# Kernel optimization log

Measured on AMD Instinct MI355X. Metric: run time of the kernel, lower is better.

## Reference

```python
import jax, jax.numpy as jnp
import numpy as np

NUM_HEADS = 8  # from init_kwargs


def setup_inputs() -> dict:
    key = jax.random.key(0)
    ks = jax.random.split(key, 8)
    B, N, Din, H, Dout, E = 4, 2048, 256, 512, 256, 65536
    s = 0.02
    return {
        "x": jax.random.normal(ks[0], (B, N, Din), jnp.float32),
        "edge_index": jax.random.randint(ks[1], (2, E), 0, N),
        "W_gcn": jax.random.normal(ks[2], (Din, H), jnp.float32) * s,
        "b_gcn": jnp.zeros((H,), jnp.float32),
        "in_proj_w": jax.random.normal(ks[3], (3 * H, H), jnp.float32) * s,
        "in_proj_b": jnp.zeros((3 * H,), jnp.float32),
        "out_proj_w": jax.random.normal(ks[4], (H, H), jnp.float32) * s,
        "out_proj_b": jnp.zeros((H,), jnp.float32),
        "fc_w": jax.random.normal(ks[5], (H, Dout), jnp.float32) * s,
        "fc_b": jnp.zeros((Dout,), jnp.float32),
    }


def _gcn(x, edge_index, W, b):
    # PyG GCNConv: add self-loops, symmetric normalization, gather-scatter aggregation.
    B, N, _ = x.shape
    loop = jnp.arange(N)
    src = jnp.concatenate([edge_index[0], loop])  # message source j
    dst = jnp.concatenate([edge_index[1], loop])  # aggregation target i
    deg = jnp.zeros((N,), x.dtype).at[dst].add(1.0)
    dinv = jnp.where(deg > 0, jax.lax.rsqrt(deg), 0.0)
    norm = dinv[src] * dinv[dst]                  # [Etot]
    xl = x @ W                                    # [B, N, H]
    msgs = xl[:, src, :] * norm[None, :, None]    # [B, Etot, H]
    out = jnp.zeros_like(xl).at[:, dst].add(msgs)  # scatter-add over edges
    return out + b


def _mha(x_nbh, wi, bi, wo, bo, nh):
    # torch MultiheadAttention, input [N(seq), B, H], self-attention.
    N, B, H = x_nbh.shape
    dh = H // nh
    qkv = x_nbh @ wi.T + bi                       # [N, B, 3H]
    q, k, v = jnp.split(qkv, 3, axis=-1)
    q = q.reshape(N, B, nh, dh) * (dh ** -0.5)
    k = k.reshape(N, B, nh, dh)
    v = v.reshape(N, B, nh, dh)
    scores = jnp.einsum("nbhd,mbhd->bhnm", q, k)  # [B, nh, N, N]
    attn = jax.nn.softmax(scores, axis=-1)
    o = jnp.einsum("bhnm,mbhd->nbhd", attn, v).reshape(N, B, H)
    return o @ wo.T + bo


def reference(x, edge_index, W_gcn, b_gcn, in_proj_w, in_proj_b,
              out_proj_w, out_proj_b, fc_w, fc_b):
    h = _gcn(x, edge_index, W_gcn, b_gcn)         # [B, N, H]
    h = jnp.transpose(h, (1, 0, 2))               # [N, B, H]
    h = _mha(h, in_proj_w, in_proj_b, out_proj_w, out_proj_b, NUM_HEADS)
    h = jnp.transpose(h, (1, 0, 2))               # [B, N, H]
    h = jax.nn.relu(h)
    return h @ fc_w + fc_b                        # [B, N, Dout]
```

## Files before the change

### kernel.cpp

```cpp
#include <hip/hip_runtime.h>
#include <hip/hip_bf16.h>


#define NN 2048
#define HH 512
#define NHEAD 8
#define DH 64

typedef _Float16 f16;
typedef __attribute__((ext_vector_type(2))) _Float16 f16x2;
typedef __attribute__((ext_vector_type(4))) _Float16 f16x4;
typedef __attribute__((ext_vector_type(8))) _Float16 f16x8;
typedef __attribute__((ext_vector_type(4))) float f32x4;

#define GLOAD_LDS16(g, l)                                              \
  __builtin_amdgcn_global_load_lds(                                    \
      (const __attribute__((address_space(1))) void*)(g),              \
      (__attribute__((address_space(3))) void*)(l), 16, 0, 0)


__global__ __launch_bounds__(256) void prep_cvt_kernel(const float* __restrict__ wi,
                                                       const float* __restrict__ wo,
                                                       f16* __restrict__ wi16,
                                                       f16* __restrict__ wo16,
                                                       float* __restrict__ deg,
                                                       int* __restrict__ cursor) {
  const int bid = blockIdx.x, t = threadIdx.x;
  if (bid < 768) {
    const int i = bid * 256 + t;
    const float4 v = ((const float4*)wi)[i];
    f16x4 o = { (f16)v.x, (f16)v.y, (f16)v.z, (f16)v.w };
    ((f16x4*)wi16)[i] = o;
  } else if (bid < 1024) {
    const int i = (bid - 768) * 256 + t;
    const float4 v = ((const float4*)wo)[i];
    f16x4 o = { (f16)v.x, (f16)v.y, (f16)v.z, (f16)v.w };
    ((f16x4*)wo16)[i] = o;
  } else {
    for (int i = t; i < NN; i += 256) { deg[i] = 1.0f; cursor[i] = 0; }
  }
}

__global__ __launch_bounds__(256) void prep_transpose_kernel(const float* __restrict__ wg,
                                                             const float* __restrict__ fcw,
                                                             f16* __restrict__ wg16t,
                                                             f16* __restrict__ fcw16t) {
  __shared__ float tbuf[32][33];
  const float* in;
  f16* outp;
  int R, C, bx, by;
  if (blockIdx.x < 128) { in = wg;  outp = wg16t;  R = 256; C = 512;
                          bx = blockIdx.x & 15; by = blockIdx.x >> 4; }
  else { int id = blockIdx.x - 128; in = fcw; outp = fcw16t; R = 512; C = 256;
         bx = id & 7; by = id >> 3; }
  const int c0 = bx * 32, r0 = by * 32;
  const int tx = threadIdx.x & 31, ty = threadIdx.x >> 5;
#pragma unroll
  for (int i = 0; i < 32; i += 8) tbuf[ty + i][tx] = in[(size_t)(r0 + ty + i) * C + c0 + tx];
  __syncthreads();
#pragma unroll
  for (int i = 0; i < 32; i += 8)
    outp[(size_t)(c0 + ty + i) * R + r0 + tx] = (f16)tbuf[tx][ty + i];
}


__global__ __launch_bounds__(256) void count_deg_kernel(const int* __restrict__ ei, int E,
                                                        float* __restrict__ deg) {
  int e = blockIdx.x * 256 + threadIdx.x;
  if (e < E) atomicAdd(&deg[ei[E + e]], 1.0f);
}

__global__ __launch_bounds__(1024) void build_rowptr_kernel(const float* __restrict__ deg,
                                                            float* __restrict__ dinv,
                                                            int* __restrict__ rowptr) {
  __shared__ int a[NN];
  __shared__ int bbuf[NN];
  const int t = threadIdx.x;
  for (int i = t; i < NN; i += 1024) {
    float dg = deg[i];
    a[i] = (int)dg - 1;
    dinv[i] = rsqrtf(dg);
  }
  __syncthreads();
  int* src = a;
  int* dst = bbuf;
  for (int off = 1; off < NN; off <<= 1) {
    for (int i = t; i < NN; i += 1024) {
      int v = src[i];
      if (i >= off) v += src[i - off];
      dst[i] = v;
    }
    __syncthreads();
    int* tmp = src; src = dst; dst = tmp;
  }
  for (int i = t; i < NN; i += 1024) rowptr[i + 1] = src[i];
  if (t == 0) rowptr[0] = 0;
}

__global__ __launch_bounds__(256) void fill_csr_kernel(const int* __restrict__ ei, int E,
                                                       const int* __restrict__ rowptr,
                                                       int* __restrict__ cursor,
                                                       int* __restrict__ csr_src) {
  int e = blockIdx.x * 256 + threadIdx.x;
  if (e < E) {
    int s = ei[e];
    int d = ei[E + e];
    int pos = atomicAdd(&cursor[d], 1);
    csr_src[rowptr[d] + pos] = s;
  }
}


template <int OUTMODE, bool BIAS, bool RELU, bool AF32, int MT = 128>
__global__ __launch_bounds__(256) void mfma_gemm_kernel(
    const void* __restrict__ Ap, const f16* __restrict__ Bt,
    const float* __restrict__ bias, void* __restrict__ Cout,
    int M, int N, int K,
    f16* __restrict__ q_out, f16* __restrict__ k_out, f16* __restrict__ v_out) {
  constexpr int MI = MT / 32;
  __shared__ f16 As[MT * 32];
  __shared__ f16 Bs[128 * 32];
  const int tid = threadIdx.x;
  const int wave = tid >> 6, lane = tid & 63;
  const int quad = lane >> 4, l16 = lane & 15;
  const int m0 = blockIdx.y * MT, n0 = blockIdx.x * 128;
  const int moff = (wave >> 1) * (MI * 16), noff = (wave & 1) * 64;

  f32x4 acc[MI][4];
#pragma unroll
  for (int i = 0; i < MI; ++i)
#pragma unroll
    for (int j = 0; j < 4; ++j) acc[i][j] = (f32x4){0.f, 0.f, 0.f, 0.f};

  const int rpw = MT / 4;
  const int srowA = rpw * wave + (lane >> 2);
  const int srowB = 32 * wave + (lane >> 2);
  const int kch = (lane & 3) * 8;
  const f16* Ag = (const f16*)Ap + (size_t)(m0 + srowA) * K + kch;
  const float* Ag32 = (const float*)Ap + (size_t)(m0 + srowA) * K + kch;
  const f16* Bg = Bt + (size_t)(n0 + srowB) * K + kch;
  f16* As_w = &As[(rpw * wave) * 32];
  f16* Bs_w = &Bs[(32 * wave) * 32];

  for (int k0 = 0; k0 < K; k0 += 32) {
    __syncthreads();
    if (AF32) {
#pragma unroll
      for (int t = 0; t < 2; ++t) {
        const float* g = Ag32 + k0 + (size_t)(16 * t) * K;
        const float4 u0 = *(const float4*)g;
        const float4 u1 = *(const float4*)(g + 4);
        f16x8 o = { (f16)u0.x, (f16)u0.y, (f16)u0.z, (f16)u0.w,
                    (f16)u1.x, (f16)u1.y, (f16)u1.z, (f16)u1.w };
        *(f16x8*)&As[(srowA + 16 * t) * 32 + kch] = o;
      }
    } else {
      GLOAD_LDS16(Ag + k0, As_w);
      if (MT == 128) GLOAD_LDS16(Ag + k0 + (size_t)16 * K, As_w + 16 * 32);
    }
    GLOAD_LDS16(Bg + k0, Bs_w);
    GLOAD_LDS16(Bg + k0 + (size_t)16 * K, Bs_w + 16 * 32);
    __syncthreads();
    f16x8 af[MI], bf[4];
#pragma unroll
    for (int m16 = 0; m16 < MI; ++m16)
      af[m16] = *(const f16x8*)&As[(moff + m16 * 16 + l16) * 32 + quad * 8];
#pragma unroll
    for (int n16 = 0; n16 < 4; ++n16)
      bf[n16] = *(const f16x8*)&Bs[(noff + n16 * 16 + l16) * 32 + quad * 8];
#pragma unroll
    for (int m16 = 0; m16 < MI; ++m16)
#pragma unroll
      for (int n16 = 0; n16 < 4; ++n16)
        acc[m16][n16] =
            __builtin_amdgcn_mfma_f32_16x16x32_f16(af[m16], bf[n16], acc[m16][n16], 0, 0, 0);
  }

  float bv[4];
#pragma unroll
  for (int n16 = 0; n16 < 4; ++n16)
    bv[n16] = BIAS ? bias[n0 + noff + n16 * 16 + l16] : 0.f;

  if (OUTMODE == 2) {
    const int hblk = (n0 >> 6) + (wave & 1);
    const int which = hblk >> 3, h = hblk & 7;
    f16* dst = (which == 0) ? q_out : (which == 1) ? k_out : v_out;
    const float scale = (which == 0) ? 0.125f : 1.0f;
#pragma unroll
    for (int m16 = 0; m16 < MI; ++m16) {
#pragma unroll
      for (int r = 0; r < 4; ++r) {
        const int m = m0 + moff + m16 * 16 + quad * 4 + r;
        const int b = m >> 11, ns = m & 2047;
        f16* row = dst + ((size_t)(b * 8 + h) * NN + ns) * DH;
#pragma unroll
        for (int n16 = 0; n16 < 4; ++n16) {
          const int d = n16 * 16 + l16;
          row[d] = (f16)((acc[m16][n16][r] + bv[n16]) * scale);
        }
      }
    }
  } else {
#pragma unroll
    for (int m16 = 0; m16 < MI; ++m16) {
#pragma unroll
      for (int r = 0; r < 4; ++r) {
        const size_t row = (size_t)(m0 + moff + m16 * 16 + quad * 4 + r) * N;
#pragma unroll
        for (int n16 = 0; n16 < 4; ++n16) {
          const int col = n0 + noff + n16 * 16 + l16;
          float v = acc[m16][n16][r] + bv[n16];
          if (RELU) v = fmaxf(v, 0.f);
          if (OUTMODE == 0) ((float*)Cout)[row + col] = v;
          else ((f16*)Cout)[row + col] = (f16)v;
        }
      }
    }
  }
}


__global__ __launch_bounds__(256) void gcn_aggregate_kernel(const f16* __restrict__ xl,
                                                            const float* __restrict__ dinv,
                                                            const int* __restrict__ rowptr,
                                                            const int* __restrict__ csr_src,
                                                            const float* __restrict__ b_gcn,
                                                            f16* __restrict__ out) {
  __shared__ int s_src[256];
  __shared__ float s_dv[256];
  const int i = blockIdx.x;
  const int tid = threadIdx.x;
  const int b = tid >> 6;
  const int f = (tid & 63) * 8;
  const float dv_i = dinv[i];
  const f16* xb = xl + (size_t)b * NN * HH;
  float acc[8];
  {
    const f16x8 self = *(const f16x8*)&xb[(size_t)i * HH + f];
#pragma unroll
    for (int c = 0; c < 8; ++c) acc[c] = (float)self[c] * dv_i;
  }
  const int beg = rowptr[i], end = rowptr[i + 1];
  for (int c0 = beg; c0 < end; c0 += 256) {
    const int cnt = min(256, end - c0);
    __syncthreads();
    if (tid < cnt) {
      int s = csr_src[c0 + tid];
      s_src[tid] = s;
      s_dv[tid] = dinv[s];
    }
    __syncthreads();
    for (int t = 0; t < cnt; ++t) {
      const f16x8 v = *(const f16x8*)&xb[(size_t)s_src[t] * HH + f];
      const float w = s_dv[t];
#pragma unroll
      for (int c = 0; c < 8; ++c) acc[c] = fmaf((float)v[c], w, acc[c]);
    }
  }
  const float4 bg0 = *(const float4*)&b_gcn[f];
  const float4 bg1 = *(const float4*)&b_gcn[f + 4];
  f16x8 o;
  o[0] = (f16)(acc[0] * dv_i + bg0.x);
  o[1] = (f16)(acc[1] * dv_i + bg0.y);
  o[2] = (f16)(acc[2] * dv_i + bg0.z);
  o[3] = (f16)(acc[3] * dv_i + bg0.w);
  o[4] = (f16)(acc[4] * dv_i + bg1.x);
  o[5] = (f16)(acc[5] * dv_i + bg1.y);
  o[6] = (f16)(acc[6] * dv_i + bg1.z);
  o[7] = (f16)(acc[7] * dv_i + bg1.w);
  *(f16x8*)&out[((size_t)b * NN + i) * HH + f] = o;
}


__global__ __launch_bounds__(256) void flash_attn_f16_kernel(const f16* __restrict__ Qb,
                                                             const f16* __restrict__ Kb,
                                                             const f16* __restrict__ Vb,
                                                             f16* __restrict__ Op,
                                                             float* __restrict__ Lp) {
  const int LDK = 72;
  const int LDV = 136;
  __shared__ f16 Ks[128 * LDK];
  __shared__ f16 Vt[64 * LDV];
  const int tid = threadIdx.x;
  const int wave = tid >> 6, lane = tid & 63;
  const int quad = lane >> 4, l16 = lane & 15;
  const int n0 = blockIdx.x * 128;
  const int bh = blockIdx.y;
  const int kh = blockIdx.z;
  const int b = bh >> 3, h = bh & 7;
  const f16* kb = Kb + (size_t)bh * NN * DH;
  const f16* vb = Vb + (size_t)bh * NN * DH;

  f16x8 aq[2][2];
#pragma unroll
  for (int g = 0; g < 2; ++g) {
    const f16* qf = Qb + ((size_t)bh * NN + n0 + (wave + 4 * g) * 16 + l16) * DH + quad * 8;
    aq[g][0] = *(const f16x8*)qf;
    aq[g][1] = *(const f16x8*)(qf + 32);
  }

  float l_part[2] = {0.f, 0.f};
  f32x4 acc_o[2][4];
#pragma unroll
  for (int g = 0; g < 2; ++g)
#pragma unroll
    for (int n16 = 0; n16 < 4; ++n16) acc_o[g][n16] = (f32x4){0.f, 0.f, 0.f, 0.f};

  const int vdg = tid & 15, jbb = tid >> 4;

  for (int kt = kh * 8; kt < kh * 8 + 8; ++kt) {
    const int k0 = kt * 128;
    __syncthreads();
#pragma unroll
    for (int i = 0; i < 4; ++i) {
      int idx = tid + 256 * i;
      int r = idx >> 3, koff = (idx & 7) * 8;
      *(f16x8*)&Ks[r * LDK + koff] = *(const f16x8*)(kb + (size_t)(k0 + r) * DH + koff);
    }
#pragma unroll
    for (int cc = 0; cc < 2; ++cc) {
      const int jb = jbb + 16 * cc;
      const int sb4 = (jb >> 3) * 32 + (jb & 3) * 8 + ((jb >> 2) & 1) * 4;
      f16x4 vv[4];
#pragma unroll
      for (int i = 0; i < 4; ++i)
        vv[i] = *(const f16x4*)(vb + (size_t)(k0 + jb * 4 + i) * DH + vdg * 4);
#pragma unroll
      for (int c = 0; c < 4; ++c) {
        f16x4 o = { vv[0][c], vv[1][c], vv[2][c], vv[3][c] };
        *(f16x4*)&Vt[(vdg * 4 + c) * LDV + sb4] = o;
      }
    }
    __syncthreads();
#pragma unroll
    for (int p = 0; p < 4; ++p) {
      f32x4 sA[2][2];
#pragma unroll
      for (int t = 0; t < 2; ++t) {
        const f16x8 ak0 = *(const f16x8*)&Ks[(p * 32 + t * 16 + l16) * LDK + quad * 8];
        const f16x8 ak1 = *(const f16x8*)&Ks[(p * 32 + t * 16 + l16) * LDK + quad * 8 + 32];
#pragma unroll
        for (int g = 0; g < 2; ++g) {
          f32x4 s = {0.f, 0.f, 0.f, 0.f};
          s = __builtin_amdgcn_mfma_f32_16x16x32_f16(ak0, aq[g][0], s, 0, 0, 0);
          s = __builtin_amdgcn_mfma_f32_16x16x32_f16(ak1, aq[g][1], s, 0, 0, 0);
          sA[g][t] = s;
        }
      }
      f16x8 bvv[4];
#pragma unroll
      for (int n16 = 0; n16 < 4; ++n16)
        bvv[n16] = *(const f16x8*)&Vt[(n16 * 16 + l16) * LDV + p * 32 + quad * 8];
#pragma unroll
      for (int g = 0; g < 2; ++g) {
        f16x8 ap;
        float sum = 0.f;
#pragma unroll
        for (int t = 0; t < 2; ++t)
#pragma unroll
          for (int r = 0; r < 4; ++r) {
            const float e = __expf(sA[g][t][r]);
            sum += e;
            ap[t * 4 + r] = (f16)e;
          }
        l_part[g] += sum;
#pragma unroll
        for (int n16 = 0; n16 < 4; ++n16)
          acc_o[g][n16] = __builtin_amdgcn_mfma_f32_16x16x32_f16(ap, bvv[n16], acc_o[g][n16], 0, 0, 0);
      }
    }
  }
  f16* ohalf = Op + (size_t)kh * 4 * NN * HH;
#pragma unroll
  for (int g = 0; g < 2; ++g) {
    float lp = l_part[g];
    lp += __shfl_xor(lp, 16);
    lp += __shfl_xor(lp, 32);
    const int qrow = n0 + (wave + 4 * g) * 16;
    if (quad == 0) Lp[(size_t)(kh * 32 + bh) * NN + qrow + l16] = lp;
    f16* obase = ohalf + ((size_t)b * NN + qrow) * HH + h * DH;
#pragma unroll
    for (int r = 0; r < 4; ++r)
#pragma unroll
      for (int n16 = 0; n16 < 4; ++n16)
        obase[(size_t)(quad * 4 + r) * HH + n16 * 16 + l16] = (f16)acc_o[g][n16][r];
  }
}

__global__ __launch_bounds__(256) void attn_combine_kernel(const f16* __restrict__ Op,
                                                           const float* __restrict__ Lp,
                                                           f16* __restrict__ attn) {
  const int idx = blockIdx.x * 256 + threadIdx.x;
  const int row = idx >> 7, c4 = (idx & 127) * 4;
  const int h = c4 >> 6;
  const int b = row >> 11, n = row & 2047;
  const int bh = b * 8 + h;
  const float l = Lp[(size_t)bh * NN + n] + Lp[(size_t)(32 + bh) * NN + n];
  const float inv = 1.0f / l;
  const f16x4 a0 = *(const f16x4*)&Op[(size_t)row * HH + c4];
  const f16x4 a1 = *(const f16x4*)&Op[(size_t)(4 * NN + row) * HH + c4];
  f16x4 o;
#pragma unroll
  for (int c = 0; c < 4; ++c) o[c] = (f16)(((float)a0[c] + (float)a1[c]) * inv);
  *(f16x4*)&attn[(size_t)row * HH + c4] = o;
}


extern "C" void kernel_launch(void* const* d_in, const int* in_sizes, int n_in,
                              void* d_out, int out_size, void* d_ws, size_t ws_size,
                              hipStream_t stream) {
  const float* x     = (const float*)d_in[0];
  const int*   ei    = (const int*)d_in[1];
  const float* W_gcn = (const float*)d_in[2];
  const float* b_gcn = (const float*)d_in[3];
  const float* wi    = (const float*)d_in[4];
  const float* bi    = (const float*)d_in[5];
  const float* wo    = (const float*)d_in[6];
  const float* bo    = (const float*)d_in[7];
  const float* fcw   = (const float*)d_in[8];
  const float* fcb   = (const float*)d_in[9];
  float* out = (float*)d_out;
  const int E = in_sizes[1] / 2;
  const int M = 4 * NN;

  char* wsb = (char*)d_ws;
  const size_t MB = 1u << 20;
  f16* xl16   = (f16*)(wsb + 4 * MB);
  f16* hb16   = (f16*)(wsb + 12 * MB);
  f16* Opart  = (f16*)(wsb + 4 * MB);
  f16* Qb     = (f16*)(wsb + 20 * MB);
  f16* Kb     = (f16*)(wsb + 28 * MB);
  f16* Vb     = (f16*)(wsb + 36 * MB);
  f16* attn16 = (f16*)(wsb + 44 * MB);
  f16* proj16 = (f16*)(wsb + 52 * MB);
  f16* wi16   = (f16*)(wsb + 60 * MB);
  f16* wo16   = (f16*)(wsb + 62 * MB);
  f16* wg16t  = (f16*)(wsb + 63 * MB);
  f16* fcw16t = (f16*)(wsb + 64 * MB);
  float* deg  = (float*)(wsb + 65 * MB);
  float* dinv = deg + NN;
  int* rowptr = (int*)(dinv + NN);
  int* cursor = rowptr + 2080;
  int* csr    = cursor + NN;
  float* Lpart = (float*)(wsb + 66 * MB);

  prep_cvt_kernel<<<1025, 256, 0, stream>>>(wi, wo, wi16, wo16, deg, cursor);
  prep_transpose_kernel<<<256, 256, 0, stream>>>(W_gcn, fcw, wg16t, fcw16t);

  count_deg_kernel<<<(E + 255) / 256, 256, 0, stream>>>(ei, E, deg);
  build_rowptr_kernel<<<1, 1024, 0, stream>>>(deg, dinv, rowptr);
  fill_csr_kernel<<<(E + 255) / 256, 256, 0, stream>>>(ei, E, rowptr, cursor, csr);

  mfma_gemm_kernel<1, false, false, true><<<dim3(4, 64), 256, 0, stream>>>(
      x, wg16t, nullptr, xl16, M, 512, 256, nullptr, nullptr, nullptr);
  gcn_aggregate_kernel<<<NN, 256, 0, stream>>>(xl16, dinv, rowptr, csr, b_gcn, hb16);
  mfma_gemm_kernel<2, true, false, false><<<dim3(12, 64), 256, 0, stream>>>(
      hb16, wi16, bi, nullptr, M, 1536, 512, Qb, Kb, Vb);
  flash_attn_f16_kernel<<<dim3(NN / 128, 32, 2), 256, 0, stream>>>(Qb, Kb, Vb, Opart, Lpart);
  attn_combine_kernel<<<M * (HH / 4) / 256, 256, 0, stream>>>(Opart, Lpart, attn16);
  mfma_gemm_kernel<1, true, true, false><<<dim3(4, 64), 256, 0, stream>>>(
      attn16, wo16, bo, proj16, M, 512, 512, nullptr, nullptr, nullptr);
  mfma_gemm_kernel<0, true, false, false, 64><<<dim3(2, 128), 256, 0, stream>>>(
      proj16, fcw16t, fcb, out, M, 256, 512, nullptr, nullptr, nullptr);
}
```

Measured before the change: 263.9 us.

## Drop attention split-K and combine kernel, use exp2 with prescaled Q, smaller GEMM tiles

The flash attention kernel no longer splits the key range into two halves. Each block loops over all keys, normalizes by the row sum itself and writes the final f16 output, so the partial-output buffer and the separate combine kernel go away. The log2(e) factor is folded into the Q scale so exp2f replaces __expf, and probabilities are packed with cvt_pkrtz. Two GEMMs switch to 64-row tiles with twice as many blocks, trading per-block reuse for more parallelism, while attention has half as many blocks, each running twice as long.

```diff
diff --git a/kernel.cpp b/kernel.cpp
--- a/kernel.cpp
+++ b/kernel.cpp
@@ -11,6 +11,7 @@
 typedef __attribute__((ext_vector_type(2))) _Float16 f16x2;
 typedef __attribute__((ext_vector_type(4))) _Float16 f16x4;
 typedef __attribute__((ext_vector_type(8))) _Float16 f16x8;
+typedef __attribute__((ext_vector_type(2))) __fp16 fp16v2;
 typedef __attribute__((ext_vector_type(4))) float f32x4;
 
 #define GLOAD_LDS16(g, l)                                              \
@@ -146,7 +147,7 @@
     __syncthreads();
     if (AF32) {
 #pragma unroll
-      for (int t = 0; t < 2; ++t) {
+      for (int t = 0; t < (MT == 128 ? 2 : 1); ++t) {
         const float* g = Ag32 + k0 + (size_t)(16 * t) * K;
         const float4 u0 = *(const float4*)g;
         const float4 u1 = *(const float4*)(g + 4);
@@ -185,7 +186,7 @@
     const int hblk = (n0 >> 6) + (wave & 1);
     const int which = hblk >> 3, h = hblk & 7;
     f16* dst = (which == 0) ? q_out : (which == 1) ? k_out : v_out;
-    const float scale = (which == 0) ? 0.125f : 1.0f;
+    const float scale = (which == 0) ? 0.125f * 1.44269504f : 1.0f;
 #pragma unroll
     for (int m16 = 0; m16 < MI; ++m16) {
 #pragma unroll
@@ -275,8 +276,7 @@
 __global__ __launch_bounds__(256) void flash_attn_f16_kernel(const f16* __restrict__ Qb,
                                                              const f16* __restrict__ Kb,
                                                              const f16* __restrict__ Vb,
-                                                             f16* __restrict__ Op,
-                                                             float* __restrict__ Lp) {
+                                                             f16* __restrict__ out) {
   const int LDK = 72;
   const int LDV = 136;
   __shared__ f16 Ks[128 * LDK];
@@ -286,7 +286,6 @@
   const int quad = lane >> 4, l16 = lane & 15;
   const int n0 = blockIdx.x * 128;
   const int bh = blockIdx.y;
-  const int kh = blockIdx.z;
   const int b = bh >> 3, h = bh & 7;
   const f16* kb = Kb + (size_t)bh * NN * DH;
   const f16* vb = Vb + (size_t)bh * NN * DH;
@@ -308,7 +307,7 @@
 
   const int vdg = tid & 15, jbb = tid >> 4;
 
-  for (int kt = kh * 8; kt < kh * 8 + 8; ++kt) {
+  for (int kt = 0; kt < NN / 128; ++kt) {
     const int k0 = kt * 128;
     __syncthreads();
 #pragma unroll
@@ -353,56 +352,42 @@
         bvv[n16] = *(const f16x8*)&Vt[(n16 * 16 + l16) * LDV + p * 32 + quad * 8];
 #pragma unroll
       for (int g = 0; g < 2; ++g) {
-        f16x8 ap;
+        float e[8];
         float sum = 0.f;
 #pragma unroll
         for (int t = 0; t < 2; ++t)
 #pragma unroll
           for (int r = 0; r < 4; ++r) {
-            const float e = __expf(sA[g][t][r]);
-            sum += e;
-            ap[t * 4 + r] = (f16)e;
+            const float v = exp2f(sA[g][t][r]);
+            e[t * 4 + r] = v;
+            sum += v;
           }
         l_part[g] += sum;
+        union { f16x8 v8; fp16v2 p2[4]; } ap;
+#pragma unroll
+        for (int c = 0; c < 4; ++c)
+          ap.p2[c] = __builtin_amdgcn_cvt_pkrtz(e[2 * c], e[2 * c + 1]);
 #pragma unroll
         for (int n16 = 0; n16 < 4; ++n16)
-          acc_o[g][n16] = __builtin_amdgcn_mfma_f32_16x16x32_f16(ap, bvv[n16], acc_o[g][n16], 0, 0, 0);
-      }
-    }
-  }
-  f16* ohalf = Op + (size_t)kh * 4 * NN * HH;
+          acc_o[g][n16] = __builtin_amdgcn_mfma_f32_16x16x32_f16(ap.v8, bvv[n16], acc_o[g][n16], 0, 0, 0);
+      }
+    }
+  }
 #pragma unroll
   for (int g = 0; g < 2; ++g) {
     float lp = l_part[g];
     lp += __shfl_xor(lp, 16);
     lp += __shfl_xor(lp, 32);
-    const int qrow = n0 + (wave + 4 * g) * 16;
-    if (quad == 0) Lp[(size_t)(kh * 32 + bh) * NN + qrow + l16] = lp;
-    f16* obase = ohalf + ((size_t)b * NN + qrow) * HH + h * DH;
-#pragma unroll
-    for (int r = 0; r < 4; ++r)
+    f16* obase = out + ((size_t)b * NN + n0 + (wave + 4 * g) * 16) * HH + h * DH;
+#pragma unroll
+    for (int r = 0; r < 4; ++r) {
+      const float lr = __shfl(lp, (lane & 48) | (quad * 4 + r));
+      const float inv = 1.0f / lr;
 #pragma unroll
       for (int n16 = 0; n16 < 4; ++n16)
-        obase[(size_t)(quad * 4 + r) * HH + n16 * 16 + l16] = (f16)acc_o[g][n16][r];
-  }
-}
-
-__global__ __launch_bounds__(256) void attn_combine_kernel(const f16* __restrict__ Op,
-                                                           const float* __restrict__ Lp,
-                                                           f16* __restrict__ attn) {
-  const int idx = blockIdx.x * 256 + threadIdx.x;
-  const int row = idx >> 7, c4 = (idx & 127) * 4;
-  const int h = c4 >> 6;
-  const int b = row >> 11, n = row & 2047;
-  const int bh = b * 8 + h;
-  const float l = Lp[(size_t)bh * NN + n] + Lp[(size_t)(32 + bh) * NN + n];
-  const float inv = 1.0f / l;
-  const f16x4 a0 = *(const f16x4*)&Op[(size_t)row * HH + c4];
-  const f16x4 a1 = *(const f16x4*)&Op[(size_t)(4 * NN + row) * HH + c4];
-  f16x4 o;
-#pragma unroll
-  for (int c = 0; c < 4; ++c) o[c] = (f16)(((float)a0[c] + (float)a1[c]) * inv);
-  *(f16x4*)&attn[(size_t)row * HH + c4] = o;
+        obase[(size_t)(quad * 4 + r) * HH + n16 * 16 + l16] = (f16)(acc_o[g][n16][r] * inv);
+    }
+  }
 }
 
 
@@ -427,7 +412,6 @@
   const size_t MB = 1u << 20;
   f16* xl16   = (f16*)(wsb + 4 * MB);
   f16* hb16   = (f16*)(wsb + 12 * MB);
-  f16* Opart  = (f16*)(wsb + 4 * MB);
   f16* Qb     = (f16*)(wsb + 20 * MB);
   f16* Kb     = (f16*)(wsb + 28 * MB);
   f16* Vb     = (f16*)(wsb + 36 * MB);
@@ -442,7 +426,6 @@
   int* rowptr = (int*)(dinv + NN);
   int* cursor = rowptr + 2080;
   int* csr    = cursor + NN;
-  float* Lpart = (float*)(wsb + 66 * MB);
 
   prep_cvt_kernel<<<1025, 256, 0, stream>>>(wi, wo, wi16, wo16, deg, cursor);
   prep_transpose_kernel<<<256, 256, 0, stream>>>(W_gcn, fcw, wg16t, fcw16t);
@@ -451,14 +434,13 @@
   build_rowptr_kernel<<<1, 1024, 0, stream>>>(deg, dinv, rowptr);
   fill_csr_kernel<<<(E + 255) / 256, 256, 0, stream>>>(ei, E, rowptr, cursor, csr);
 
-  mfma_gemm_kernel<1, false, false, true><<<dim3(4, 64), 256, 0, stream>>>(
+  mfma_gemm_kernel<1, false, false, true, 64><<<dim3(4, 128), 256, 0, stream>>>(
       x, wg16t, nullptr, xl16, M, 512, 256, nullptr, nullptr, nullptr);
   gcn_aggregate_kernel<<<NN, 256, 0, stream>>>(xl16, dinv, rowptr, csr, b_gcn, hb16);
   mfma_gemm_kernel<2, true, false, false><<<dim3(12, 64), 256, 0, stream>>>(
       hb16, wi16, bi, nullptr, M, 1536, 512, Qb, Kb, Vb);
-  flash_attn_f16_kernel<<<dim3(NN / 128, 32, 2), 256, 0, stream>>>(Qb, Kb, Vb, Opart, Lpart);
-  attn_combine_kernel<<<M * (HH / 4) / 256, 256, 0, stream>>>(Opart, Lpart, attn16);
-  mfma_gemm_kernel<1, true, true, false><<<dim3(4, 64), 256, 0, stream>>>(
+  flash_attn_f16_kernel<<<dim3(NN / 128, 32), 256, 0, stream>>>(Qb, Kb, Vb, attn16);
+  mfma_gemm_kernel<1, true, true, false, 64><<<dim3(4, 128), 256, 0, stream>>>(
       attn16, wo16, bo, proj16, M, 512, 512, nullptr, nullptr, nullptr);
   mfma_gemm_kernel<0, true, false, false, 64><<<dim3(2, 128), 256, 0, stream>>>(
       proj16, fcw16t, fcb, out, M, 256, 512, nullptr, nullptr, nullptr);
```

New measurement: 262.0 us. Within noise of the previous version (-0.7%).
